# Performance work log

Measured on AMD Instinct MI355X. Metric: run time of the kernel, lower is better.

The kernel has to match this reference:

```python
import jax, jax.numpy as jnp
import numpy as np
from jax import lax

KS = 21      # ksize
SCALE = 4    # downscale stride


def _conv(x, w, b=None, padding='SAME'):
    # x: NCHW, w: OIHW
    y = lax.conv_general_dilated(x, w, (1, 1), padding,
                                 dimension_numbers=('NCHW', 'OIHW', 'NCHW'))
    if b is not None:
        y = y + b[None, :, None, None]
    return y


def _deg_kernel_net(z, conv0_w, conv0_b, res_w1, res_b1, res_w2, res_b2, last_w, last_b):
    # conv3x3 -> nb EDSR ResBlocks (conv-relu-conv + residual) -> conv1x1 to ksize^2
    h = _conv(z, conv0_w, conv0_b)
    for i in range(res_w1.shape[0]):  # fixed small layer count
        r = _conv(jax.nn.relu(_conv(h, res_w1[i], res_b1[i])), res_w2[i], res_b2[i])
        h = h + r
    return _conv(h, last_w, last_b)  # (B, ksize^2, H', W')


def setup_inputs() -> dict:
    key = jax.random.key(0)
    ks = jax.random.split(key, 10)
    B, C, H, W = 8, 3, 256, 256
    nf, nb, k2 = 64, 8, KS * KS
    s = 0.05  # keep activations tame through 8 residual blocks
    return {
        'x': jax.random.normal(ks[0], (B, C, H, W), jnp.float32),
        'z': jax.random.normal(ks[1], (B, C, H // SCALE, W // SCALE), jnp.float32),
        'conv0_w': jax.random.normal(ks[2], (nf, C, 3, 3), jnp.float32) * s,
        'conv0_b': jax.random.normal(ks[3], (nf,), jnp.float32) * s,
        'res_w1': jax.random.normal(ks[4], (nb, nf, nf, 3, 3), jnp.float32) * s,
        'res_b1': jax.random.normal(ks[5], (nb, nf), jnp.float32) * s,
        'res_w2': jax.random.normal(ks[6], (nb, nf, nf, 3, 3), jnp.float32) * s,
        'res_b2': jax.random.normal(ks[7], (nb, nf), jnp.float32) * s,
        'last_w': jax.random.normal(ks[8], (k2, nf, 1, 1), jnp.float32) * s,
        'last_b': jax.random.normal(ks[9], (k2,), jnp.float32) * s,
    }


def reference(x, z, conv0_w, conv0_b, res_w1, res_b1, res_w2, res_b2, last_w, last_b):
    B, C, H, W = x.shape
    hz, wz = z.shape[2], z.shape[3]
    k2 = KS * KS

    # spatially-varying kernel, normalized over the ksize^2 taps
    kernel = _deg_kernel_net(z, conv0_w, conv0_b, res_w1, res_b1,
                             res_w2, res_b2, last_w, last_b)
    kernel = kernel.reshape(B, 1, k2, hz, wz)
    kernel = kernel / (kernel.sum(axis=2, keepdims=True) + 1e-8)

    # reflection pad then unfold (im2col) with stride = scale
    p = KS // 2
    xp = jnp.pad(x.reshape(B * C, 1, H, W), ((0, 0), (0, 0), (p, p), (p, p)),
                 mode='reflect')
    patches = lax.conv_general_dilated_patches(
        xp, (KS, KS), (SCALE, SCALE), 'VALID',
        dimension_numbers=('NCHW', 'OIHW', 'NCHW'))  # (B*C, k2, hz, wz)
    patches = patches.reshape(B, C, k2, hz, wz)

    out = (patches * kernel).sum(axis=2)  # (B, C, hz, wz)
    return out, kernel.reshape(B, k2, hz, wz)
```

## Files before the change

### kernel.cpp

```cpp
#include <hip/hip_runtime.h>


#define NB 8
#define NF 64
#define SP 4096
#define PS 66
#define PS2 4356
#define K2 441
#define K2P 448
#define RES_WSTRIDE (64*64*9)
#define WF_RES 36864
#define WF_C0  1792
#define WTA_N  28672

typedef double vdbl4 __attribute__((ext_vector_type(4)));

#define T_AI 0
#define T_AK 64
#define T_BK 128
#define T_BJ 192
#define T_DI 256
#define T_DJ 512

__global__ void probe_mfma(double* __restrict__ probe)
{
    int l = threadIdx.x;
    vdbl4 z = {0.0, 0.0, 0.0, 0.0};
    vdbl4 r1 = __builtin_amdgcn_mfma_f64_16x16x4f64((double)l, 1.0, z, 0, 0, 0);
    vdbl4 r2 = __builtin_amdgcn_mfma_f64_16x16x4f64(1.0, (double)l, z, 0, 0, 0);
#pragma unroll
    for (int r = 0; r < 4; ++r) {
        probe[r * 64 + l]       = r1[r];
        probe[256 + r * 64 + l] = r2[r];
    }
}

__global__ void decode_probe(const double* __restrict__ probe, int* __restrict__ tabs)
{
    int t = threadIdx.x;
    const double* d1 = probe;
    const double* d2 = probe + 256;
    bool fA = ((((int)d1[0]) & 3) == 0);
    bool fB = ((((int)d2[0]) & 3) == 0);
    int v1 = (int)d1[t], v2 = (int)d2[t];
    tabs[T_DI + t] = fA ? (v1 - 96) >> 2 : (v1 - 6) >> 4;
    tabs[T_DJ + t] = fB ? (v2 - 96) >> 2 : (v2 - 6) >> 4;
    if (t < 64) {
        tabs[T_AI + t] = fA ? (t & 15) : (t >> 2);
        tabs[T_AK + t] = fA ? (t >> 4) : (t & 3);
        tabs[T_BK + t] = fB ? (t >> 4) : (t & 3);
        tabs[T_BJ + t] = fB ? (t & 15) : (t >> 2);
    }
}

__global__ void prep_zpad(const float* __restrict__ z, double* __restrict__ zp)
{
    int i = blockIdx.x * blockDim.x + threadIdx.x;
    if (i >= NB * 3 * SP) return;
    int bc = i >> 12, p = i & 4095, y = p >> 6, x = p & 63;
    zp[(size_t)(bc * PS + y + 1) * PS + x + 1] = (double)z[i];
}

__global__ void prep_convw_frag(const float* __restrict__ src, double* __restrict__ dst,
                                const int* __restrict__ tabs,
                                int CIN, int nlayer, int wstride)
{
    int i = blockIdx.x * blockDim.x + threadIdx.x;
    int NS = (CIN * 9 + 3) / 4;
    int M  = NS * 256;
    if (i >= nlayer * M) return;
    int li  = i / M;
    int rem = i - li * M;
    int t   = rem >> 8;
    int j   = rem & 255;
    int mt  = j >> 6;
    int l   = j & 63;
    int kg  = t * 4 + tabs[T_AK + l];
    int oc  = mt * 16 + tabs[T_AI + l];
    int c   = kg / 9;
    int tap = kg - c * 9;
    dst[i] = (kg < CIN * 9) ? (double)src[li * wstride + (oc * CIN + c) * 9 + tap] : 0.0;
}

__global__ void prep_bias_frag(const float* __restrict__ src, double* __restrict__ dst,
                               const int* __restrict__ tabs, int nlayer)
{
    int i = blockIdx.x * blockDim.x + threadIdx.x;
    if (i >= nlayer * 1024) return;
    int li  = i >> 10;
    int j   = i & 1023;
    int mtr = j >> 6;
    int l   = j & 63;
    int mt  = mtr >> 2, r = mtr & 3;
    dst[i] = (double)src[li * 64 + mt * 16 + tabs[T_DI + r * 64 + l]];
}

__global__ void prep_lastwa(const float* __restrict__ lw, const float* __restrict__ lb,
                            const int* __restrict__ tabs,
                            double* __restrict__ wta, double* __restrict__ lbp)
{
    int i = blockIdx.x * blockDim.x + threadIdx.x;
    if (i < WTA_N) {
        int kk = i / (28 * 64);
        int rem = i - kk * (28 * 64);
        int mt = rem >> 6;
        int l  = rem & 63;
        int c  = kk * 4 + tabs[T_AK + l];
        int T  = mt * 16 + tabs[T_AI + l];
        wta[i] = (T < K2) ? (double)lw[T * 64 + c] : 0.0;
    }
    if (i < K2P) lbp[i] = (i < K2) ? (double)lb[i] : 0.0;
}

__global__ void prep_wsum(const float* __restrict__ lw, const float* __restrict__ lb,
                          double* __restrict__ wsum)
{
    int c = threadIdx.x;
    if (c < 64) {
        double s = 0.0;
        for (int t = 0; t < K2; ++t) s += (double)lw[t * 64 + c];
        wsum[c] = s;
    }
    if (c == 64) {
        double s = 0.0;
        for (int t = 0; t < K2; ++t) s += (double)lb[t];
        wsum[64] = s;
    }
}

template<int CIN, bool RELU, bool RESADD>
__global__ __launch_bounds__(256, 2)
void conv3x3_mfma(const double* __restrict__ in, const double* __restrict__ WF,
                  const double* __restrict__ BF, const int* __restrict__ tabs,
                  const double* __restrict__ res, double* __restrict__ out)
{
    constexpr int KT = CIN * 9;
    constexpr int NS = (KT + 3) / 4;
    constexpr int G  = (NS + 8) / 9;

    const int bid = blockIdx.x;
    const int b   = bid & 7;
    const int y0  = bid >> 3;
    const int tid = threadIdx.x;
    const int w   = tid >> 6;
    const int l   = tid & 63;
    const int mi  = w >> 1, ni = w & 1;
    const int mt0 = mi * 2, nt0 = ni * 2;

    const int kB = tabs[T_BK + l];
    const int jB = tabs[T_BJ + l];

    int offp[9];
#pragma unroll
    for (int s = 0; s < 9; ++s) {
        int kg  = s * 4 + kB;
        int off = 0;
        if (KT >= 36 || kg < KT) {
            int c   = kg / 9;
            int tap = kg - c * 9;
            int dy  = tap / 3, dx = tap - dy * 3;
            off = c * PS2 + dy * PS + dx;
        }
        offp[s] = off + jB + nt0 * 16;
    }

    const double* bbase = in + (size_t)b * CIN * PS2 + (size_t)y0 * PS;

    vdbl4 acc[2][2];
#pragma unroll
    for (int mt = 0; mt < 2; ++mt)
#pragma unroll
        for (int r = 0; r < 4; ++r) {
            double bv = BF[((mt0 + mt) * 4 + r) * 64 + l];
            acc[mt][0][r] = bv;
            acc[mt][1][r] = bv;
        }

    double aS[3][2], bS[3][2];
    auto ldA = [&](int t, int slot) {
        const double* p = WF + (size_t)t * 256 + l;
        aS[slot][0] = p[mt0 * 64];
        aS[slot][1] = p[(mt0 + 1) * 64];
    };
    auto ldB = [&](size_t cg, int s, int slot) {
        const double* p = bbase + cg + offp[s];
        bS[slot][0] = p[0];
        bS[slot][1] = p[16];
    };
    auto step = [&](int slot) {
        acc[0][0] = __builtin_amdgcn_mfma_f64_16x16x4f64(aS[slot][0], bS[slot][0], acc[0][0], 0, 0, 0);
        acc[0][1] = __builtin_amdgcn_mfma_f64_16x16x4f64(aS[slot][0], bS[slot][1], acc[0][1], 0, 0, 0);
        acc[1][0] = __builtin_amdgcn_mfma_f64_16x16x4f64(aS[slot][1], bS[slot][0], acc[1][0], 0, 0, 0);
        acc[1][1] = __builtin_amdgcn_mfma_f64_16x16x4f64(aS[slot][1], bS[slot][1], acc[1][1], 0, 0, 0);
    };

    ldA(0, 0); ldB(0, 0, 0);
    ldA(1, 1); ldB(0, 1, 1);

    for (int g = 0; g < G; ++g) {
        const size_t cg = (size_t)g * 4 * PS2;
#pragma unroll
        for (int s = 0; s < 9; ++s) {
            const int t = g * 9 + s;
            if (KT % 36 != 0 && t >= NS) break;
            const int tp = t + 2;
            if (tp < NS) {
                const int    ps  = (s + 2 < 9) ? s + 2 : s - 7;
                const size_t pcg = (s + 2 < 9) ? cg : cg + 4 * PS2;
                ldA(tp, (s + 2) % 3);
                ldB(pcg, ps, (s + 2) % 3);
            }
            step(s % 3);
        }
    }

    int iD[4], jD[4];
#pragma unroll
    for (int r = 0; r < 4; ++r) {
        iD[r] = tabs[T_DI + r * 64 + l];
        jD[r] = tabs[T_DJ + r * 64 + l];
    }
#pragma unroll
    for (int mt = 0; mt < 2; ++mt)
#pragma unroll
        for (int nt = 0; nt < 2; ++nt)
#pragma unroll
            for (int r = 0; r < 4; ++r) {
                int oc = (mt0 + mt) * 16 + iD[r];
                int x  = (nt0 + nt) * 16 + jD[r];
                size_t idx = (size_t)(b * NF + oc) * PS2 + (size_t)(y0 + 1) * PS + x + 1;
                double val = acc[mt][nt][r];
                if (RELU)   val = fmax(val, 0.0);
                if (RESADD) val += res[idx];
                out[idx] = val;
            }
}

__global__ __launch_bounds__(256, 2)
void lastconv_mfma(const double* __restrict__ hp, const double* __restrict__ wta,
                   const double* __restrict__ lbp, const int* __restrict__ tabs,
                   float* __restrict__ kraw)
{
    const int b   = blockIdx.x >> 6;
    const int row = blockIdx.x & 63;
    const int tid = threadIdx.x;
    const int w   = tid >> 6;
    const int l   = tid & 63;

    const int kB = tabs[T_BK + l];
    const int jB = tabs[T_BJ + l];
    int iD[4], jD[4];
#pragma unroll
    for (int r = 0; r < 4; ++r) {
        iD[r] = tabs[T_DI + r * 64 + l];
        jD[r] = tabs[T_DJ + r * 64 + l];
    }

    const double* hbase = hp + (size_t)b * NF * PS2 + (size_t)(row + 1) * PS + 1;
    float* kbase = kraw + (size_t)b * K2 * SP + row * 64;
    const int mt0 = w * 7;

    for (int nt = 0; nt < 4; ++nt) {
        vdbl4 acc[7];
#pragma unroll
        for (int n = 0; n < 7; ++n)
#pragma unroll
            for (int r = 0; r < 4; ++r)
                acc[n][r] = lbp[(mt0 + n) * 16 + iD[r]];

        double bv = hbase[(size_t)kB * PS2 + nt * 16 + jB];
        for (int kk = 0; kk < 16; ++kk) {
            double nb = 0.0;
            if (kk < 15)
                nb = hbase[(size_t)((kk + 1) * 4 + kB) * PS2 + nt * 16 + jB];
            const double* ap = wta + ((size_t)kk * 28 + mt0) * 64 + l;
#pragma unroll
            for (int n = 0; n < 7; ++n)
                acc[n] = __builtin_amdgcn_mfma_f64_16x16x4f64(ap[n * 64], bv, acc[n], 0, 0, 0);
            bv = nb;
        }

#pragma unroll
        for (int n = 0; n < 7; ++n)
#pragma unroll
            for (int r = 0; r < 4; ++r) {
                int T = (mt0 + n) * 16 + iD[r];
                if (T < K2)
                    kbase[(size_t)T * SP + nt * 16 + jD[r]] = (float)acc[n][r];
            }
    }
}

__global__ __launch_bounds__(256)
void sums_kernel(const double* __restrict__ hp, const double* __restrict__ wsum,
                 double* __restrict__ sums)
{
    int i = blockIdx.x * 256 + threadIdx.x;
    int b = i >> 12, p = i & 4095;
    int y = p >> 6, x = p & 63;
    const double* hb = hp + (size_t)b * NF * PS2 + (size_t)(y + 1) * PS + 1 + x;
    double s = wsum[64];
    for (int c = 0; c < 64; ++c) s += hb[(size_t)c * PS2] * wsum[c];
    sums[b * SP + p] = s;
}

__global__ __launch_bounds__(256)
void apply_kernel(const float* __restrict__ x, const double* __restrict__ sums,
                  float* __restrict__ kout, float* __restrict__ out)
{
    const int bid  = blockIdx.x;
    const int g    = bid & 3;
    const int tile = (bid >> 2) & 15;
    const int b    = bid >> 6;
    const int i0   = (tile >> 2) << 4;
    const int j0   = (tile & 3) << 4;
    const int tid  = threadIdx.x;
    const int ti   = tid >> 4, tj = tid & 15;

    __shared__ float s_x[3][81][84];

    for (int e = tid; e < 3 * 81 * 84; e += 256) {
        int c   = e / 6804;
        int rem = e - c * 6804;
        int u   = rem / 84;
        int v   = rem - u * 84;
        int gr  = i0 * 4 + u - 10;
        int gc  = j0 * 4 + v - 10;
        gr = gr < 0 ? -gr : (gr > 255 ? 510 - gr : gr);
        gc = gc < 0 ? -gc : (gc > 255 ? 510 - gc : gc);
        int vp = (v & 3) * 21 + (v >> 2);
        s_x[c][u][vp] = x[((b * 3 + c) * 256 + gr) * 256 + gc];
    }
    __syncthreads();

    const int p = (i0 + ti) * 64 + (j0 + tj);
    const double inv = 1.0 / (sums[b * SP + p] + 1e-8);

    float o0 = 0.f, o1 = 0.f, o2 = 0.f;
    const int t0 = g * 111;
    const int t1 = (t0 + 111 < K2) ? t0 + 111 : K2;
    for (int t = t0; t < t1; ++t) {
        int ty = t / 21, tx = t - ty * 21;
        float* kp = &kout[(size_t)(b * K2 + t) * SP + p];
        float k  = *kp;
        float kn = (float)((double)k * inv);
        *kp = kn;
        int u  = ti * 4 + ty;
        int vp = (tx & 3) * 21 + tj + (tx >> 2);
        o0 = fmaf(s_x[0][u][vp], kn, o0);
        o1 = fmaf(s_x[1][u][vp], kn, o1);
        o2 = fmaf(s_x[2][u][vp], kn, o2);
    }
    atomicAdd(&out[(b * 3 + 0) * SP + p], o0);
    atomicAdd(&out[(b * 3 + 1) * SP + p], o1);
    atomicAdd(&out[(b * 3 + 2) * SP + p], o2);
}

extern "C" void kernel_launch(void* const* d_in, const int* in_sizes, int n_in,
                              void* d_out, int out_size, void* d_ws, size_t ws_size,
                              hipStream_t stream)
{
    (void)in_sizes; (void)n_in; (void)out_size; (void)ws_size;

    const float* x = (const float*)d_in[0];
    const float* z = (const float*)d_in[1];

    float* out  = (float*)d_out;
    float* kout = (float*)d_out + NB * 3 * SP;

    double* wd    = (double*)d_ws;
    double* probe = wd;
    int*    tabs  = (int*)(wd + 512);
    double* wf0   = wd + 1024;
    double* wf1   = wf0 + WF_C0;
    double* wf2   = wf1 + 8 * WF_RES;
    double* bf0   = wf2 + 8 * WF_RES;
    double* bf1   = bf0 + 1024;
    double* bf2   = bf1 + 8 * 1024;
    double* wta   = bf2 + 8 * 1024;
    double* lbp   = wta + WTA_N;
    double* wsum  = lbp + K2P;
    double* zp    = wsum + 72;
    double* hp    = zp + NB * 3 * PS2;
    double* tp    = hp + NB * NF * PS2;
    double* sums  = tp;

    hipMemsetAsync(zp, 0, (size_t)NB * 3 * PS2 * sizeof(double), stream);
    hipMemsetAsync(hp, 0, (size_t)NB * NF * PS2 * sizeof(double), stream);
    hipMemsetAsync(tp, 0, (size_t)NB * NF * PS2 * sizeof(double), stream);
    hipMemsetAsync(out, 0, NB * 3 * SP * sizeof(float), stream);

    probe_mfma<<<1, 64, 0, stream>>>(probe);
    decode_probe<<<1, 256, 0, stream>>>(probe, tabs);

    prep_zpad<<<(NB * 3 * SP + 255) / 256, 256, 0, stream>>>(z, zp);
    prep_convw_frag<<<(WF_C0 + 255) / 256, 256, 0, stream>>>(
        (const float*)d_in[2], wf0, tabs, 3, 1, 0);
    prep_convw_frag<<<(8 * WF_RES + 255) / 256, 256, 0, stream>>>(
        (const float*)d_in[4], wf1, tabs, 64, 8, RES_WSTRIDE);
    prep_convw_frag<<<(8 * WF_RES + 255) / 256, 256, 0, stream>>>(
        (const float*)d_in[6], wf2, tabs, 64, 8, RES_WSTRIDE);
    prep_bias_frag<<<(1024 + 255) / 256, 256, 0, stream>>>(
        (const float*)d_in[3], bf0, tabs, 1);
    prep_bias_frag<<<(8 * 1024 + 255) / 256, 256, 0, stream>>>(
        (const float*)d_in[5], bf1, tabs, 8);
    prep_bias_frag<<<(8 * 1024 + 255) / 256, 256, 0, stream>>>(
        (const float*)d_in[7], bf2, tabs, 8);
    prep_lastwa<<<(WTA_N + 255) / 256, 256, 0, stream>>>(
        (const float*)d_in[8], (const float*)d_in[9], tabs, wta, lbp);
    prep_wsum<<<1, 128, 0, stream>>>(
        (const float*)d_in[8], (const float*)d_in[9], wsum);

    conv3x3_mfma<3,  false, false><<<512, 256, 0, stream>>>(zp, wf0, bf0, tabs, nullptr, hp);
    for (int i = 0; i < 8; ++i) {
        conv3x3_mfma<64, true,  false><<<512, 256, 0, stream>>>(
            hp, wf1 + i * WF_RES, bf1 + i * 1024, tabs, nullptr, tp);
        conv3x3_mfma<64, false, true ><<<512, 256, 0, stream>>>(
            tp, wf2 + i * WF_RES, bf2 + i * 1024, tabs, hp, hp);
    }
    sums_kernel<<<128, 256, 0, stream>>>(hp, wsum, sums);
    lastconv_mfma<<<512, 256, 0, stream>>>(hp, wta, lbp, tabs, kout);
    apply_kernel<<<512, 256, 0, stream>>>(x, sums, kout, out);
}
```

Baseline: 1.011 ms.

## Restructure last 1x1 conv to keep weight fragments in registers per wave

The last 1x1 conv kernel is retiled so that each wave owns one 16-row output tile of the 441-tap kernel and holds all 16 of its weight fragments in registers. It then loops over 8 row chunks of pixels with 4 MFMA accumulators each. This replaces the old scheme, where each block handled one image row and every wave reloaded 7 weight tiles from global memory for each 16-pixel sub-tile. The grid drops from 512 to 448 blocks. In exchange, activation reads are repeated across the 7 tile groups, and output stores now cover 64 consecutive pixels per row.

```diff
diff --git a/kernel.cpp b/kernel.cpp
--- a/kernel.cpp
+++ b/kernel.cpp
@@ -241,11 +241,15 @@
                    const double* __restrict__ lbp, const int* __restrict__ tabs,
                    float* __restrict__ kraw)
 {
-    const int b   = blockIdx.x >> 6;
-    const int row = blockIdx.x & 63;
+    const int bid = blockIdx.x;
+    const int b   = bid / 56;
+    const int rem = bid - b * 56;
+    const int tg  = rem >> 3;
+    const int pc  = rem & 7;
     const int tid = threadIdx.x;
     const int w   = tid >> 6;
     const int l   = tid & 63;
+    const int mt  = tg * 4 + w;
 
     const int kB = tabs[T_BK + l];
     const int jB = tabs[T_BJ + l];
@@ -256,38 +260,60 @@
         jD[r] = tabs[T_DJ + r * 64 + l];
     }
 
-    const double* hbase = hp + (size_t)b * NF * PS2 + (size_t)(row + 1) * PS + 1;
-    float* kbase = kraw + (size_t)b * K2 * SP + row * 64;
-    const int mt0 = w * 7;
-
-    for (int nt = 0; nt < 4; ++nt) {
-        vdbl4 acc[7];
-#pragma unroll
-        for (int n = 0; n < 7; ++n)
+    double avs[16];
+#pragma unroll
+    for (int kk = 0; kk < 16; ++kk)
+        avs[kk] = wta[((size_t)kk * 28 + mt) * 64 + l];
+
+    double bias[4];
+#pragma unroll
+    for (int r = 0; r < 4; ++r)
+        bias[r] = lbp[mt * 16 + iD[r]];
+
+    const double* hb = hp + (size_t)b * NF * PS2;
+    float* kb = kraw + (size_t)b * K2 * SP;
+
+    for (int q = 0; q < 8; ++q) {
+        const int P0  = pc * 512 + q * 64;
+        const int row = P0 >> 6;
+        const double* hrow = hb + (size_t)(row + 1) * PS + 1 + jB;
+
+        vdbl4 acc[4];
+#pragma unroll
+        for (int j = 0; j < 4; ++j)
 #pragma unroll
             for (int r = 0; r < 4; ++r)
-                acc[n][r] = lbp[(mt0 + n) * 16 + iD[r]];
-
-        double bv = hbase[(size_t)kB * PS2 + nt * 16 + jB];
+                acc[j][r] = bias[r];
+
+        double bc[4], bn[4];
+#pragma unroll
+        for (int j = 0; j < 4; ++j)
+            bc[j] = hrow[(size_t)kB * PS2 + j * 16];
+
         for (int kk = 0; kk < 16; ++kk) {
-            double nb = 0.0;
-            if (kk < 15)
-                nb = hbase[(size_t)((kk + 1) * 4 + kB) * PS2 + nt * 16 + jB];
-            const double* ap = wta + ((size_t)kk * 28 + mt0) * 64 + l;
-#pragma unroll
-            for (int n = 0; n < 7; ++n)
-                acc[n] = __builtin_amdgcn_mfma_f64_16x16x4f64(ap[n * 64], bv, acc[n], 0, 0, 0);
-            bv = nb;
+            if (kk < 15) {
+                const double* np = hrow + (size_t)((kk + 1) * 4 + kB) * PS2;
+#pragma unroll
+                for (int j = 0; j < 4; ++j) bn[j] = np[j * 16];
+            }
+#pragma unroll
+            for (int j = 0; j < 4; ++j)
+                acc[j] = __builtin_amdgcn_mfma_f64_16x16x4f64(avs[kk], bc[j], acc[j], 0, 0, 0);
+#pragma unroll
+            for (int j = 0; j < 4; ++j) bc[j] = bn[j];
         }
 
 #pragma unroll
-        for (int n = 0; n < 7; ++n)
-#pragma unroll
-            for (int r = 0; r < 4; ++r) {
-                int T = (mt0 + n) * 16 + iD[r];
-                if (T < K2)
-                    kbase[(size_t)T * SP + nt * 16 + jD[r]] = (float)acc[n][r];
+        for (int r = 0; r < 4; ++r) {
+            int T = mt * 16 + iD[r];
+            if (T < K2) {
+                float* p = kb + (size_t)T * SP + P0;
+                p[jD[r]]      = (float)acc[0][r];
+                p[16 + jD[r]] = (float)acc[1][r];
+                p[32 + jD[r]] = (float)acc[2][r];
+                p[48 + jD[r]] = (float)acc[3][r];
             }
+        }
     }
 }
 
@@ -419,6 +445,6 @@
             tp, wf2 + i * WF_RES, bf2 + i * 1024, tabs, hp, hp);
     }
     sums_kernel<<<128, 256, 0, stream>>>(hp, wsum, sums);
-    lastconv_mfma<<<512, 256, 0, stream>>>(hp, wta, lbp, tabs, kout);
+    lastconv_mfma<<<448, 256, 0, stream>>>(hp, wta, lbp, tabs, kout);
     apply_kernel<<<512, 256, 0, stream>>>(x, sums, kout, out);
 }
```

New measurement: 1.012 ms. No clear change (+0.1%).
